# Optimization experiments

Hardware: AMD Instinct MI355X
Metric: run time of the kernel (lower is better)

Reference implementation:

```python
import jax, jax.numpy as jnp
import numpy as np

N_F = 256
NH = 8
D = N_F // NH
TP = (2.0 * D) ** 0.5  # temperature: sqrt(temperature_coeff * d)
N_A = 4096


def setup_inputs() -> dict:
    key = jax.random.key(0)
    ks = jax.random.split(key, 8)
    s = 1.0 / np.sqrt(N_F)
    x = jax.random.normal(ks[0], (1, N_A, N_F), dtype=jnp.float32)
    batch_mask = jax.random.randint(ks[1], (N_A, N_A), 0, 2) > 0  # bool
    Wq = jax.random.normal(ks[2], (N_F, N_F), dtype=jnp.float32) * s
    bq = jax.random.normal(ks[3], (N_F,), dtype=jnp.float32) * s
    Wk = jax.random.normal(ks[4], (N_F, N_F), dtype=jnp.float32) * s
    bk = jax.random.normal(ks[5], (N_F,), dtype=jnp.float32) * s
    Wv = jax.random.normal(ks[6], (N_F, N_F), dtype=jnp.float32) * s
    bv = jax.random.normal(ks[7], (N_F,), dtype=jnp.float32) * s
    return {"x": x, "batch_mask": batch_mask, "Wq": Wq, "bq": bq,
            "Wk": Wk, "bk": bk, "Wv": Wv, "bv": bv}


def reference(x, batch_mask, Wq, bq, Wk, bk, Wv, bv):
    # x: (1, n_a, n_f). torch Linear: y = x @ W.T + b
    n_a = x.shape[1]
    q = (x @ Wq.T + bq).reshape(n_a, NH, D)  # (n_a, nh, d)
    k = (x @ Wk.T + bk).reshape(n_a, NH, D)
    v = (x @ Wv.T + bv).reshape(n_a, NH, D)
    # scores: (nh, n_a, n_a)
    a = jnp.einsum('qhd,khd->hqk', q, k) / TP
    neg = jnp.finfo(a.dtype).min
    a = jnp.where(batch_mask[None, :, :], neg, a)
    alpha = jax.nn.softmax(a, axis=-1)
    out = jnp.einsum('hqk,khd->qhd', alpha, v).reshape(1, n_a, NH * D)
    return out
```

## Files before the change

### kernel.cpp

```cpp
#include <hip/hip_runtime.h>
#include <hip/hip_fp16.h>
#include <cfloat>

#define NA 4096
#define NF 256
#define NH 8
#define DH 32
#define KSPLIT 4
#define CHUNK (NA / KSPLIT)

typedef _Float16 half8_t __attribute__((ext_vector_type(8)));
typedef _Float16 half4_t __attribute__((ext_vector_type(4)));
typedef float f32x4 __attribute__((ext_vector_type(4)));
typedef unsigned long long u64;
typedef unsigned long long u64x2 __attribute__((ext_vector_type(2)));

#define QSCALE 0.1803368800112723f

__global__ __launch_bounds__(256) void cast_kernel(
    const float* __restrict__ x, const float* __restrict__ wq,
    const float* __restrict__ wk, const float* __restrict__ wv,
    _Float16* __restrict__ xh, _Float16* __restrict__ whq,
    _Float16* __restrict__ whk, _Float16* __restrict__ whv) {
  const int XQ = NA * NF / 4;
  const int WQ = NF * NF / 4;
  int i = blockIdx.x * blockDim.x + threadIdx.x;
  const float* src; _Float16* dst; int q;
  if (i < XQ)               { src = x;  dst = xh;  q = i; }
  else if (i < XQ + WQ)     { src = wq; dst = whq; q = i - XQ; }
  else if (i < XQ + 2 * WQ) { src = wk; dst = whk; q = i - XQ - WQ; }
  else if (i < XQ + 3 * WQ) { src = wv; dst = whv; q = i - XQ - 2 * WQ; }
  else return;
  float4 v = *(const float4*)(src + q * 4);
  half4_t h = { (_Float16)v.x, (_Float16)v.y, (_Float16)v.z, (_Float16)v.w };
  *(half4_t*)(dst + q * 4) = h;
}

__global__ __launch_bounds__(512) void pack_mask(
    const int* __restrict__ mask, u64* __restrict__ pm) {
  const int q = blockIdx.x * 8 + (threadIdx.x >> 6);
  const int lane = threadIdx.x & 63;
  const int4* rowv = (const int4*)(mask + (size_t)q * NA);
  u64* dst = pm + (size_t)q * 64;
  for (int G = 0; G < 16; ++G) {
    int4 v = rowv[G * 64 + lane];
    u64 b0 = __ballot(v.x != 0);
    u64 b1 = __ballot(v.y != 0);
    u64 b2 = __ballot(v.z != 0);
    u64 b3 = __ballot(v.w != 0);
    if (lane == 0) {
      u64x2 lo = { b0, b1 };
      u64x2 hi = { b2, b3 };
      *(u64x2*)(dst + G * 4) = lo;
      *(u64x2*)(dst + G * 4 + 2) = hi;
    }
  }
}

__global__ __launch_bounds__(256) void proj_gemm(
    const _Float16* __restrict__ xh,
    const _Float16* __restrict__ whq, const _Float16* __restrict__ whk,
    const _Float16* __restrict__ whv,
    const float* __restrict__ bq, const float* __restrict__ bk,
    const float* __restrict__ bv,
    _Float16* __restrict__ Qh, _Float16* __restrict__ Kh,
    _Float16* __restrict__ Vt) {
  const int wave = threadIdx.x >> 6;
  const int lane = threadIdx.x & 63;
  const int lr = lane & 15;
  const int lg = lane >> 4;
  const int lg4 = lg * 4;
  const int m0 = blockIdx.x * 16;
  const int mat = blockIdx.y >> 2;
  const int n0 = (blockIdx.y & 3) * 64 + wave * 16;
  const _Float16* W = (mat == 0) ? whq : (mat == 1) ? whk : whv;
  const float* bias = (mat == 0) ? bq : (mat == 1) ? bk : bv;

  f32x4 acc = {0.f, 0.f, 0.f, 0.f};
#pragma unroll
  for (int k0 = 0; k0 < NF; k0 += 32) {
    half8_t afrag = *(const half8_t*)(xh + (m0 + lr) * NF + k0 + lg * 8);
    half8_t bfrag = *(const half8_t*)(W + (n0 + lr) * NF + k0 + lg * 8);
    acc = __builtin_amdgcn_mfma_f32_16x16x32_f16(afrag, bfrag, acc, 0, 0, 0);
  }
  const int n = n0 + lr;
  const float b = bias[n];
  const int hh = n >> 5;
  const int dd = n & 31;
  if (mat == 0) {
#pragma unroll
    for (int j = 0; j < 4; j++)
      Qh[((size_t)hh * NA + m0 + lg4 + j) * DH + dd] =
          (_Float16)((acc[j] + b) * QSCALE);
  } else if (mat == 1) {
#pragma unroll
    for (int j = 0; j < 4; j++)
      Kh[((size_t)hh * NA + m0 + lg4 + j) * DH + dd] =
          (_Float16)(acc[j] + b);
  } else {
    half4_t hv = { (_Float16)(acc[0] + b), (_Float16)(acc[1] + b),
                   (_Float16)(acc[2] + b), (_Float16)(acc[3] + b) };
    *(half4_t*)(Vt + (size_t)n * NA + m0 + lg4) = hv;
  }
}

__global__ __launch_bounds__(512) void attn_kernel(
    const _Float16* __restrict__ Qh, const _Float16* __restrict__ Kh,
    const _Float16* __restrict__ Vt, const u64* __restrict__ pm,
    float* __restrict__ part, float* __restrict__ sbuf) {
  __shared__ _Float16 vlds[256 * 64];
  const int tid = threadIdx.x;
  const int h = tid >> 6;
  const int lane = tid & 63;
  const int lq = lane & 15;
  const int lg = lane >> 4;
  const int q0 = blockIdx.x * 16;
  const int kb = blockIdx.y;
  const int k0 = kb * CHUNK;

  const half8_t qfrag = *(const half8_t*)(Qh + ((size_t)h * NA + q0 + lq) * DH + lg * 8);
  const _Float16* Kb = Kh + ((size_t)h * NA + k0) * DH;
  const u64* pmq = pm + (size_t)(q0 + lq) * 64 + kb * 16;

  const int str = tid >> 3;
  const int gx = (tid & 7) ^ (str & 7);
  const _Float16* Vp0 = Vt + (size_t)str * NA + k0 + gx * 8;
  const int wr = str * 64 + (tid & 7) * 8;

  int ro[2][4];
#pragma unroll
  for (int u = 0; u < 2; ++u)
#pragma unroll
    for (int t = 0; t < 4; ++t)
      ro[u][t] = (h * DH + u * 16 + lq) * 64 +
                 (((2 * t + (lg >> 1)) ^ (lq & 7)) << 3) + (lg & 1) * 4;

  const int sh0 = lg, sh1 = lg + 4, sh2 = lg + 8, sh3 = lg + 12;

  f32x4 z = {0.f, 0.f, 0.f, 0.f};
  f32x4 o0 = z, o1 = z;
  float srun = 0.f;

  for (int Gc = 0; Gc < 4; ++Gc) {
    const u64* wp = pmq + Gc * 4;
    u64x2 wa = *(const u64x2*)wp;
    u64x2 wb = *(const u64x2*)(wp + 2);
    const u64 w0 = wa[0], w1 = wa[1], w2 = wb[0], w3 = wb[1];
#pragma unroll
    for (int s = 0; s < 4; ++s) {
      const int kt = Gc * 256 + s * 64;
      half8_t vg0 = *(const half8_t*)(Vp0 + kt);
      half8_t vg1 = *(const half8_t*)(Vp0 + (size_t)64 * NA + kt);
      half8_t vg2 = *(const half8_t*)(Vp0 + (size_t)128 * NA + kt);
      half8_t vg3 = *(const half8_t*)(Vp0 + (size_t)192 * NA + kt);

      half8_t kf0 = *(const half8_t*)(Kb + (size_t)(kt + 0 * 16 + lq) * DH + lg * 8);
      half8_t kf1 = *(const half8_t*)(Kb + (size_t)(kt + 1 * 16 + lq) * DH + lg * 8);
      half8_t kf2 = *(const half8_t*)(Kb + (size_t)(kt + 2 * 16 + lq) * DH + lg * 8);
      half8_t kf3 = *(const half8_t*)(Kb + (size_t)(kt + 3 * 16 + lq) * DH + lg * 8);
      f32x4 st0 = __builtin_amdgcn_mfma_f32_16x16x32_f16(kf0, qfrag, z, 0, 0, 0);
      f32x4 st1 = __builtin_amdgcn_mfma_f32_16x16x32_f16(kf1, qfrag, z, 0, 0, 0);
      f32x4 st2 = __builtin_amdgcn_mfma_f32_16x16x32_f16(kf2, qfrag, z, 0, 0, 0);
      f32x4 st3 = __builtin_amdgcn_mfma_f32_16x16x32_f16(kf3, qfrag, z, 0, 0, 0);

      const unsigned m0s = (unsigned)(w0 >> (16 * s));
      const unsigned m1s = (unsigned)(w1 >> (16 * s));
      const unsigned m2s = (unsigned)(w2 >> (16 * s));
      const unsigned m3s = (unsigned)(w3 >> (16 * s));

      f32x4 e0, e1, e2, e3;
      e0[0] = ((m0s >> sh0) & 1) ? 0.f : __builtin_exp2f(st0[0]);
      e0[1] = ((m1s >> sh0) & 1) ? 0.f : __builtin_exp2f(st0[1]);
      e0[2] = ((m2s >> sh0) & 1) ? 0.f : __builtin_exp2f(st0[2]);
      e0[3] = ((m3s >> sh0) & 1) ? 0.f : __builtin_exp2f(st0[3]);
      e1[0] = ((m0s >> sh1) & 1) ? 0.f : __builtin_exp2f(st1[0]);
      e1[1] = ((m1s >> sh1) & 1) ? 0.f : __builtin_exp2f(st1[1]);
      e1[2] = ((m2s >> sh1) & 1) ? 0.f : __builtin_exp2f(st1[2]);
      e1[3] = ((m3s >> sh1) & 1) ? 0.f : __builtin_exp2f(st1[3]);
      e2[0] = ((m0s >> sh2) & 1) ? 0.f : __builtin_exp2f(st2[0]);
      e2[1] = ((m1s >> sh2) & 1) ? 0.f : __builtin_exp2f(st2[1]);
      e2[2] = ((m2s >> sh2) & 1) ? 0.f : __builtin_exp2f(st2[2]);
      e2[3] = ((m3s >> sh2) & 1) ? 0.f : __builtin_exp2f(st2[3]);
      e3[0] = ((m0s >> sh3) & 1) ? 0.f : __builtin_exp2f(st3[0]);
      e3[1] = ((m1s >> sh3) & 1) ? 0.f : __builtin_exp2f(st3[1]);
      e3[2] = ((m2s >> sh3) & 1) ? 0.f : __builtin_exp2f(st3[2]);
      e3[3] = ((m3s >> sh3) & 1) ? 0.f : __builtin_exp2f(st3[3]);

      srun += (e0[0] + e0[1] + e0[2] + e0[3]) + (e1[0] + e1[1] + e1[2] + e1[3])
            + (e2[0] + e2[1] + e2[2] + e2[3]) + (e3[0] + e3[1] + e3[2] + e3[3]);

      half4_t pt0 = { (_Float16)e0[0], (_Float16)e0[1], (_Float16)e0[2], (_Float16)e0[3] };
      half4_t pt1 = { (_Float16)e1[0], (_Float16)e1[1], (_Float16)e1[2], (_Float16)e1[3] };
      half4_t pt2 = { (_Float16)e2[0], (_Float16)e2[1], (_Float16)e2[2], (_Float16)e2[3] };
      half4_t pt3 = { (_Float16)e3[0], (_Float16)e3[1], (_Float16)e3[2], (_Float16)e3[3] };

      *(half8_t*)&vlds[wr]         = vg0;
      *(half8_t*)&vlds[wr + 4096]  = vg1;
      *(half8_t*)&vlds[wr + 8192]  = vg2;
      *(half8_t*)&vlds[wr + 12288] = vg3;
      __syncthreads();

      half4_t va, vb;
      va = *(const half4_t*)&vlds[ro[0][0]]; vb = *(const half4_t*)&vlds[ro[1][0]];
      o0 = __builtin_amdgcn_mfma_f32_16x16x16f16(va, pt0, o0, 0, 0, 0);
      o1 = __builtin_amdgcn_mfma_f32_16x16x16f16(vb, pt0, o1, 0, 0, 0);
      va = *(const half4_t*)&vlds[ro[0][1]]; vb = *(const half4_t*)&vlds[ro[1][1]];
      o0 = __builtin_amdgcn_mfma_f32_16x16x16f16(va, pt1, o0, 0, 0, 0);
      o1 = __builtin_amdgcn_mfma_f32_16x16x16f16(vb, pt1, o1, 0, 0, 0);
      va = *(const half4_t*)&vlds[ro[0][2]]; vb = *(const half4_t*)&vlds[ro[1][2]];
      o0 = __builtin_amdgcn_mfma_f32_16x16x16f16(va, pt2, o0, 0, 0, 0);
      o1 = __builtin_amdgcn_mfma_f32_16x16x16f16(vb, pt2, o1, 0, 0, 0);
      va = *(const half4_t*)&vlds[ro[0][3]]; vb = *(const half4_t*)&vlds[ro[1][3]];
      o0 = __builtin_amdgcn_mfma_f32_16x16x16f16(va, pt3, o0, 0, 0, 0);
      o1 = __builtin_amdgcn_mfma_f32_16x16x16f16(vb, pt3, o1, 0, 0, 0);
      __syncthreads();
    }
  }

  srun += __shfl_xor(srun, 16);
  srun += __shfl_xor(srun, 32);

  const int pb = (blockIdx.x * KSPLIT + kb) * NH + h;
  float* pp = part + (size_t)pb * 512 + lane * 8;
  float4 w0v = { o0[0], o0[1], o0[2], o0[3] };
  float4 w1v = { o1[0], o1[1], o1[2], o1[3] };
  *(float4*)(pp) = w0v;
  *(float4*)(pp + 4) = w1v;
  if (lg == 0) sbuf[pb * 16 + lq] = srun;
}

__global__ __launch_bounds__(256) void combine_kernel(
    const float* __restrict__ part, const float* __restrict__ sbuf,
    float* __restrict__ out) {
  const int wave = blockIdx.x * 4 + (threadIdx.x >> 6);
  const int qt = wave >> 3;
  const int h = wave & 7;
  const int lane = threadIdx.x & 63;
  const int lq = lane & 15;
  const int lg = lane >> 4;

  float S = 0.f;
  float4 O0 = {0.f, 0.f, 0.f, 0.f}, O1 = {0.f, 0.f, 0.f, 0.f};
#pragma unroll
  for (int kb = 0; kb < KSPLIT; kb++) {
    const int pb = (qt * KSPLIT + kb) * NH + h;
    float4 a0 = *(const float4*)(part + (size_t)pb * 512 + lane * 8);
    float4 a1 = *(const float4*)(part + (size_t)pb * 512 + lane * 8 + 4);
    S += sbuf[pb * 16 + lq];
    O0.x += a0.x; O0.y += a0.y; O0.z += a0.z; O0.w += a0.w;
    O1.x += a1.x; O1.y += a1.y; O1.z += a1.z; O1.w += a1.w;
  }
  const float inv = 1.f / S;
  float* orow = out + (qt * 16 + lq) * NF + h * DH;
  float4 r0 = { O0.x * inv, O0.y * inv, O0.z * inv, O0.w * inv };
  float4 r1 = { O1.x * inv, O1.y * inv, O1.z * inv, O1.w * inv };
  *(float4*)(orow + lg * 4) = r0;
  *(float4*)(orow + 16 + lg * 4) = r1;
}

extern "C" void kernel_launch(void* const* d_in, const int* in_sizes, int n_in,
                              void* d_out, int out_size, void* d_ws, size_t ws_size,
                              hipStream_t stream) {
  const float* x  = (const float*)d_in[0];
  const int* mask = (const int*)d_in[1];
  const float* Wq = (const float*)d_in[2];
  const float* bq = (const float*)d_in[3];
  const float* Wk = (const float*)d_in[4];
  const float* bk = (const float*)d_in[5];
  const float* Wv = (const float*)d_in[6];
  const float* bv = (const float*)d_in[7];
  float* out = (float*)d_out;

  char* ws = (char*)d_ws;
  _Float16* xh = (_Float16*)(ws + 0);
  u64* pm      = (u64*)(ws + 0);
  _Float16* whq = (_Float16*)(ws + 2097152);
  _Float16* whk = (_Float16*)(ws + 2228224);
  _Float16* whv = (_Float16*)(ws + 2359296);
  _Float16* Qh  = (_Float16*)(ws + 2490368);
  _Float16* Kh  = (_Float16*)(ws + 4587520);
  _Float16* Vt  = (_Float16*)(ws + 6684672);
  float* part   = (float*)(ws + 8781824);
  float* sbuf   = (float*)(ws + 25559040);

  cast_kernel<<<1216, 256, 0, stream>>>(x, Wq, Wk, Wv, xh, whq, whk, whv);
  proj_gemm<<<dim3(256, 12), 256, 0, stream>>>(xh, whq, whk, whv, bq, bk, bv,
                                               Qh, Kh, Vt);
  pack_mask<<<512, 512, 0, stream>>>(mask, pm);
  attn_kernel<<<dim3(NA / 16, KSPLIT), 512, 0, stream>>>(Qh, Kh, Vt, pm,
                                                         part, sbuf);
  combine_kernel<<<512, 256, 0, stream>>>(part, sbuf, out);
}
```

Measured before the change: 221.2 us.

## Process two query tiles per attention block and fuse fp16 cast into projection

```diff
diff --git a/kernel.cpp b/kernel.cpp
--- a/kernel.cpp
+++ b/kernel.cpp
@@ -8,33 +8,16 @@
 #define DH 32
 #define KSPLIT 4
 #define CHUNK (NA / KSPLIT)
+#define QBLK 32
 
 typedef _Float16 half8_t __attribute__((ext_vector_type(8)));
 typedef _Float16 half4_t __attribute__((ext_vector_type(4)));
 typedef float f32x4 __attribute__((ext_vector_type(4)));
+typedef float f32x8 __attribute__((ext_vector_type(8)));
 typedef unsigned long long u64;
 typedef unsigned long long u64x2 __attribute__((ext_vector_type(2)));
 
 #define QSCALE 0.1803368800112723f
-
-__global__ __launch_bounds__(256) void cast_kernel(
-    const float* __restrict__ x, const float* __restrict__ wq,
-    const float* __restrict__ wk, const float* __restrict__ wv,
-    _Float16* __restrict__ xh, _Float16* __restrict__ whq,
-    _Float16* __restrict__ whk, _Float16* __restrict__ whv) {
-  const int XQ = NA * NF / 4;
-  const int WQ = NF * NF / 4;
-  int i = blockIdx.x * blockDim.x + threadIdx.x;
-  const float* src; _Float16* dst; int q;
-  if (i < XQ)               { src = x;  dst = xh;  q = i; }
-  else if (i < XQ + WQ)     { src = wq; dst = whq; q = i - XQ; }
-  else if (i < XQ + 2 * WQ) { src = wk; dst = whk; q = i - XQ - WQ; }
-  else if (i < XQ + 3 * WQ) { src = wv; dst = whv; q = i - XQ - 2 * WQ; }
-  else return;
-  float4 v = *(const float4*)(src + q * 4);
-  half4_t h = { (_Float16)v.x, (_Float16)v.y, (_Float16)v.z, (_Float16)v.w };
-  *(half4_t*)(dst + q * 4) = h;
-}
 
 __global__ __launch_bounds__(512) void pack_mask(
     const int* __restrict__ mask, u64* __restrict__ pm) {
@@ -58,29 +41,31 @@
 }
 
 __global__ __launch_bounds__(256) void proj_gemm(
-    const _Float16* __restrict__ xh,
-    const _Float16* __restrict__ whq, const _Float16* __restrict__ whk,
-    const _Float16* __restrict__ whv,
+    const float* __restrict__ x,
+    const float* __restrict__ wq, const float* __restrict__ wk,
+    const float* __restrict__ wv,
     const float* __restrict__ bq, const float* __restrict__ bk,
     const float* __restrict__ bv,
     _Float16* __restrict__ Qh, _Float16* __restrict__ Kh,
     _Float16* __restrict__ Vt) {
-  const int wave = threadIdx.x >> 6;
   const int lane = threadIdx.x & 63;
   const int lr = lane & 15;
   const int lg = lane >> 4;
   const int lg4 = lg * 4;
   const int m0 = blockIdx.x * 16;
   const int mat = blockIdx.y >> 2;
-  const int n0 = (blockIdx.y & 3) * 64 + wave * 16;
-  const _Float16* W = (mat == 0) ? whq : (mat == 1) ? whk : whv;
+  const int n0 = (blockIdx.y & 3) * 64 + (threadIdx.x >> 6) * 16;
+  const float* W = (mat == 0) ? wq : (mat == 1) ? wk : wv;
   const float* bias = (mat == 0) ? bq : (mat == 1) ? bk : bv;
 
   f32x4 acc = {0.f, 0.f, 0.f, 0.f};
 #pragma unroll
   for (int k0 = 0; k0 < NF; k0 += 32) {
-    half8_t afrag = *(const half8_t*)(xh + (m0 + lr) * NF + k0 + lg * 8);
-    half8_t bfrag = *(const half8_t*)(W + (n0 + lr) * NF + k0 + lg * 8);
+    f32x8 af = *(const f32x8*)(x + (size_t)(m0 + lr) * NF + k0 + lg * 8);
+    f32x8 bf = *(const f32x8*)(W + (size_t)(n0 + lr) * NF + k0 + lg * 8);
+    half8_t afrag, bfrag;
+#pragma unroll
+    for (int i = 0; i < 8; ++i) { afrag[i] = (_Float16)af[i]; bfrag[i] = (_Float16)bf[i]; }
     acc = __builtin_amdgcn_mfma_f32_16x16x32_f16(afrag, bfrag, acc, 0, 0, 0);
   }
   const int n = n0 + lr;
@@ -104,7 +89,7 @@
   }
 }
 
-__global__ __launch_bounds__(512) void attn_kernel(
+__global__ __launch_bounds__(512, 4) void attn_kernel(
     const _Float16* __restrict__ Qh, const _Float16* __restrict__ Kh,
     const _Float16* __restrict__ Vt, const u64* __restrict__ pm,
     float* __restrict__ part, float* __restrict__ sbuf) {
@@ -114,13 +99,15 @@
   const int lane = tid & 63;
   const int lq = lane & 15;
   const int lg = lane >> 4;
-  const int q0 = blockIdx.x * 16;
+  const int q0 = blockIdx.x * QBLK;
   const int kb = blockIdx.y;
   const int k0 = kb * CHUNK;
 
-  const half8_t qfrag = *(const half8_t*)(Qh + ((size_t)h * NA + q0 + lq) * DH + lg * 8);
+  const half8_t qfA = *(const half8_t*)(Qh + ((size_t)h * NA + q0 + lq) * DH + lg * 8);
+  const half8_t qfB = *(const half8_t*)(Qh + ((size_t)h * NA + q0 + 16 + lq) * DH + lg * 8);
   const _Float16* Kb = Kh + ((size_t)h * NA + k0) * DH;
-  const u64* pmq = pm + (size_t)(q0 + lq) * 64 + kb * 16;
+  const u64* pmA = pm + (size_t)(q0 + lq) * 64 + kb * 16;
+  const u64* pmB = pm + (size_t)(q0 + 16 + lq) * 64 + kb * 16;
 
   const int str = tid >> 3;
   const int gx = (tid & 7) ^ (str & 7);
@@ -138,14 +125,14 @@
   const int sh0 = lg, sh1 = lg + 4, sh2 = lg + 8, sh3 = lg + 12;
 
   f32x4 z = {0.f, 0.f, 0.f, 0.f};
-  f32x4 o0 = z, o1 = z;
-  float srun = 0.f;
+  f32x4 oA0 = z, oA1 = z, oB0 = z, oB1 = z;
+  float srA = 0.f, srB = 0.f;
 
   for (int Gc = 0; Gc < 4; ++Gc) {
-    const u64* wp = pmq + Gc * 4;
-    u64x2 wa = *(const u64x2*)wp;
-    u64x2 wb = *(const u64x2*)(wp + 2);
-    const u64 w0 = wa[0], w1 = wa[1], w2 = wb[0], w3 = wb[1];
+    u64x2 waA = *(const u64x2*)(pmA + Gc * 4);
+    u64x2 wbA = *(const u64x2*)(pmA + Gc * 4 + 2);
+    u64x2 waB = *(const u64x2*)(pmB + Gc * 4);
+    u64x2 wbB = *(const u64x2*)(pmB + Gc * 4 + 2);
 #pragma unroll
     for (int s = 0; s < 4; ++s) {
       const int kt = Gc * 256 + s * 64;
@@ -158,41 +145,71 @@
       half8_t kf1 = *(const half8_t*)(Kb + (size_t)(kt + 1 * 16 + lq) * DH + lg * 8);
       half8_t kf2 = *(const half8_t*)(Kb + (size_t)(kt + 2 * 16 + lq) * DH + lg * 8);
       half8_t kf3 = *(const half8_t*)(Kb + (size_t)(kt + 3 * 16 + lq) * DH + lg * 8);
-      f32x4 st0 = __builtin_amdgcn_mfma_f32_16x16x32_f16(kf0, qfrag, z, 0, 0, 0);
-      f32x4 st1 = __builtin_amdgcn_mfma_f32_16x16x32_f16(kf1, qfrag, z, 0, 0, 0);
-      f32x4 st2 = __builtin_amdgcn_mfma_f32_16x16x32_f16(kf2, qfrag, z, 0, 0, 0);
-      f32x4 st3 = __builtin_amdgcn_mfma_f32_16x16x32_f16(kf3, qfrag, z, 0, 0, 0);
-
-      const unsigned m0s = (unsigned)(w0 >> (16 * s));
-      const unsigned m1s = (unsigned)(w1 >> (16 * s));
-      const unsigned m2s = (unsigned)(w2 >> (16 * s));
-      const unsigned m3s = (unsigned)(w3 >> (16 * s));
-
-      f32x4 e0, e1, e2, e3;
-      e0[0] = ((m0s >> sh0) & 1) ? 0.f : __builtin_exp2f(st0[0]);
-      e0[1] = ((m1s >> sh0) & 1) ? 0.f : __builtin_exp2f(st0[1]);
-      e0[2] = ((m2s >> sh0) & 1) ? 0.f : __builtin_exp2f(st0[2]);
-      e0[3] = ((m3s >> sh0) & 1) ? 0.f : __builtin_exp2f(st0[3]);
-      e1[0] = ((m0s >> sh1) & 1) ? 0.f : __builtin_exp2f(st1[0]);
-      e1[1] = ((m1s >> sh1) & 1) ? 0.f : __builtin_exp2f(st1[1]);
-      e1[2] = ((m2s >> sh1) & 1) ? 0.f : __builtin_exp2f(st1[2]);
-      e1[3] = ((m3s >> sh1) & 1) ? 0.f : __builtin_exp2f(st1[3]);
-      e2[0] = ((m0s >> sh2) & 1) ? 0.f : __builtin_exp2f(st2[0]);
-      e2[1] = ((m1s >> sh2) & 1) ? 0.f : __builtin_exp2f(st2[1]);
-      e2[2] = ((m2s >> sh2) & 1) ? 0.f : __builtin_exp2f(st2[2]);
-      e2[3] = ((m3s >> sh2) & 1) ? 0.f : __builtin_exp2f(st2[3]);
-      e3[0] = ((m0s >> sh3) & 1) ? 0.f : __builtin_exp2f(st3[0]);
-      e3[1] = ((m1s >> sh3) & 1) ? 0.f : __builtin_exp2f(st3[1]);
-      e3[2] = ((m2s >> sh3) & 1) ? 0.f : __builtin_exp2f(st3[2]);
-      e3[3] = ((m3s >> sh3) & 1) ? 0.f : __builtin_exp2f(st3[3]);
-
-      srun += (e0[0] + e0[1] + e0[2] + e0[3]) + (e1[0] + e1[1] + e1[2] + e1[3])
-            + (e2[0] + e2[1] + e2[2] + e2[3]) + (e3[0] + e3[1] + e3[2] + e3[3]);
-
-      half4_t pt0 = { (_Float16)e0[0], (_Float16)e0[1], (_Float16)e0[2], (_Float16)e0[3] };
-      half4_t pt1 = { (_Float16)e1[0], (_Float16)e1[1], (_Float16)e1[2], (_Float16)e1[3] };
-      half4_t pt2 = { (_Float16)e2[0], (_Float16)e2[1], (_Float16)e2[2], (_Float16)e2[3] };
-      half4_t pt3 = { (_Float16)e3[0], (_Float16)e3[1], (_Float16)e3[2], (_Float16)e3[3] };
+      f32x4 sA0 = __builtin_amdgcn_mfma_f32_16x16x32_f16(kf0, qfA, z, 0, 0, 0);
+      f32x4 sA1 = __builtin_amdgcn_mfma_f32_16x16x32_f16(kf1, qfA, z, 0, 0, 0);
+      f32x4 sA2 = __builtin_amdgcn_mfma_f32_16x16x32_f16(kf2, qfA, z, 0, 0, 0);
+      f32x4 sA3 = __builtin_amdgcn_mfma_f32_16x16x32_f16(kf3, qfA, z, 0, 0, 0);
+      f32x4 sB0 = __builtin_amdgcn_mfma_f32_16x16x32_f16(kf0, qfB, z, 0, 0, 0);
+      f32x4 sB1 = __builtin_amdgcn_mfma_f32_16x16x32_f16(kf1, qfB, z, 0, 0, 0);
+      f32x4 sB2 = __builtin_amdgcn_mfma_f32_16x16x32_f16(kf2, qfB, z, 0, 0, 0);
+      f32x4 sB3 = __builtin_amdgcn_mfma_f32_16x16x32_f16(kf3, qfB, z, 0, 0, 0);
+
+      const unsigned mA0 = (unsigned)(waA[0] >> (16 * s));
+      const unsigned mA1 = (unsigned)(waA[1] >> (16 * s));
+      const unsigned mA2 = (unsigned)(wbA[0] >> (16 * s));
+      const unsigned mA3 = (unsigned)(wbA[1] >> (16 * s));
+      const unsigned mB0 = (unsigned)(waB[0] >> (16 * s));
+      const unsigned mB1 = (unsigned)(waB[1] >> (16 * s));
+      const unsigned mB2 = (unsigned)(wbB[0] >> (16 * s));
+      const unsigned mB3 = (unsigned)(wbB[1] >> (16 * s));
+
+      f32x4 eA0, eA1, eA2, eA3, eB0, eB1, eB2, eB3;
+      eA0[0] = ((mA0 >> sh0) & 1) ? 0.f : __builtin_exp2f(sA0[0]);
+      eA0[1] = ((mA1 >> sh0) & 1) ? 0.f : __builtin_exp2f(sA0[1]);
+      eA0[2] = ((mA2 >> sh0) & 1) ? 0.f : __builtin_exp2f(sA0[2]);
+      eA0[3] = ((mA3 >> sh0) & 1) ? 0.f : __builtin_exp2f(sA0[3]);
+      eA1[0] = ((mA0 >> sh1) & 1) ? 0.f : __builtin_exp2f(sA1[0]);
+      eA1[1] = ((mA1 >> sh1) & 1) ? 0.f : __builtin_exp2f(sA1[1]);
+      eA1[2] = ((mA2 >> sh1) & 1) ? 0.f : __builtin_exp2f(sA1[2]);
+      eA1[3] = ((mA3 >> sh1) & 1) ? 0.f : __builtin_exp2f(sA1[3]);
+      eA2[0] = ((mA0 >> sh2) & 1) ? 0.f : __builtin_exp2f(sA2[0]);
+      eA2[1] = ((mA1 >> sh2) & 1) ? 0.f : __builtin_exp2f(sA2[1]);
+      eA2[2] = ((mA2 >> sh2) & 1) ? 0.f : __builtin_exp2f(sA2[2]);
+      eA2[3] = ((mA3 >> sh2) & 1) ? 0.f : __builtin_exp2f(sA2[3]);
+      eA3[0] = ((mA0 >> sh3) & 1) ? 0.f : __builtin_exp2f(sA3[0]);
+      eA3[1] = ((mA1 >> sh3) & 1) ? 0.f : __builtin_exp2f(sA3[1]);
+      eA3[2] = ((mA2 >> sh3) & 1) ? 0.f : __builtin_exp2f(sA3[2]);
+      eA3[3] = ((mA3 >> sh3) & 1) ? 0.f : __builtin_exp2f(sA3[3]);
+      eB0[0] = ((mB0 >> sh0) & 1) ? 0.f : __builtin_exp2f(sB0[0]);
+      eB0[1] = ((mB1 >> sh0) & 1) ? 0.f : __builtin_exp2f(sB0[1]);
+      eB0[2] = ((mB2 >> sh0) & 1) ? 0.f : __builtin_exp2f(sB0[2]);
+      eB0[3] = ((mB3 >> sh0) & 1) ? 0.f : __builtin_exp2f(sB0[3]);
+      eB1[0] = ((mB0 >> sh1) & 1) ? 0.f : __builtin_exp2f(sB1[0]);
+      eB1[1] = ((mB1 >> sh1) & 1) ? 0.f : __builtin_exp2f(sB1[1]);
+      eB1[2] = ((mB2 >> sh1) & 1) ? 0.f : __builtin_exp2f(sB1[2]);
+      eB1[3] = ((mB3 >> sh1) & 1) ? 0.f : __builtin_exp2f(sB1[3]);
+      eB2[0] = ((mB0 >> sh2) & 1) ? 0.f : __builtin_exp2f(sB2[0]);
+      eB2[1] = ((mB1 >> sh2) & 1) ? 0.f : __builtin_exp2f(sB2[1]);
+      eB2[2] = ((mB2 >> sh2) & 1) ? 0.f : __builtin_exp2f(sB2[2]);
+      eB2[3] = ((mB3 >> sh2) & 1) ? 0.f : __builtin_exp2f(sB2[3]);
+      eB3[0] = ((mB0 >> sh3) & 1) ? 0.f : __builtin_exp2f(sB3[0]);
+      eB3[1] = ((mB1 >> sh3) & 1) ? 0.f : __builtin_exp2f(sB3[1]);
+      eB3[2] = ((mB2 >> sh3) & 1) ? 0.f : __builtin_exp2f(sB3[2]);
+      eB3[3] = ((mB3 >> sh3) & 1) ? 0.f : __builtin_exp2f(sB3[3]);
+
+      srA += (eA0[0] + eA0[1] + eA0[2] + eA0[3]) + (eA1[0] + eA1[1] + eA1[2] + eA1[3])
+           + (eA2[0] + eA2[1] + eA2[2] + eA2[3]) + (eA3[0] + eA3[1] + eA3[2] + eA3[3]);
+      srB += (eB0[0] + eB0[1] + eB0[2] + eB0[3]) + (eB1[0] + eB1[1] + eB1[2] + eB1[3])
+           + (eB2[0] + eB2[1] + eB2[2] + eB2[3]) + (eB3[0] + eB3[1] + eB3[2] + eB3[3]);
+
+      half4_t pA0 = { (_Float16)eA0[0], (_Float16)eA0[1], (_Float16)eA0[2], (_Float16)eA0[3] };
+      half4_t pA1 = { (_Float16)eA1[0], (_Float16)eA1[1], (_Float16)eA1[2], (_Float16)eA1[3] };
+      half4_t pA2 = { (_Float16)eA2[0], (_Float16)eA2[1], (_Float16)eA2[2], (_Float16)eA2[3] };
+      half4_t pA3 = { (_Float16)eA3[0], (_Float16)eA3[1], (_Float16)eA3[2], (_Float16)eA3[3] };
+      half4_t pB0 = { (_Float16)eB0[0], (_Float16)eB0[1], (_Float16)eB0[2], (_Float16)eB0[3] };
+      half4_t pB1 = { (_Float16)eB1[0], (_Float16)eB1[1], (_Float16)eB1[2], (_Float16)eB1[3] };
+      half4_t pB2 = { (_Float16)eB2[0], (_Float16)eB2[1], (_Float16)eB2[2], (_Float16)eB2[3] };
+      half4_t pB3 = { (_Float16)eB3[0], (_Float16)eB3[1], (_Float16)eB3[2], (_Float16)eB3[3] };
 
       *(half8_t*)&vlds[wr]         = vg0;
       *(half8_t*)&vlds[wr + 4096]  = vg1;
@@ -202,31 +219,42 @@
 
       half4_t va, vb;
       va = *(const half4_t*)&vlds[ro[0][0]]; vb = *(const half4_t*)&vlds[ro[1][0]];
-      o0 = __builtin_amdgcn_mfma_f32_16x16x16f16(va, pt0, o0, 0, 0, 0);
-      o1 = __builtin_amdgcn_mfma_f32_16x16x16f16(vb, pt0, o1, 0, 0, 0);
+      oA0 = __builtin_amdgcn_mfma_f32_16x16x16f16(va, pA0, oA0, 0, 0, 0);
+      oA1 = __builtin_amdgcn_mfma_f32_16x16x16f16(vb, pA0, oA1, 0, 0, 0);
+      oB0 = __builtin_amdgcn_mfma_f32_16x16x16f16(va, pB0, oB0, 0, 0, 0);
+      oB1 = __builtin_amdgcn_mfma_f32_16x16x16f16(vb, pB0, oB1, 0, 0, 0);
       va = *(const half4_t*)&vlds[ro[0][1]]; vb = *(const half4_t*)&vlds[ro[1][1]];
-      o0 = __builtin_amdgcn_mfma_f32_16x16x16f16(va, pt1, o0, 0, 0, 0);
-      o1 = __builtin_amdgcn_mfma_f32_16x16x16f16(vb, pt1, o1, 0, 0, 0);
+      oA0 = __builtin_amdgcn_mfma_f32_16x16x16f16(va, pA1, oA0, 0, 0, 0);
+      oA1 = __builtin_amdgcn_mfma_f32_16x16x16f16(vb, pA1, oA1, 0, 0, 0);
+      oB0 = __builtin_amdgcn_mfma_f32_16x16x16f16(va, pB1, oB0, 0, 0, 0);
+      oB1 = __builtin_amdgcn_mfma_f32_16x16x16f16(vb, pB1, oB1, 0, 0, 0);
       va = *(const half4_t*)&vlds[ro[0][2]]; vb = *(const half4_t*)&vlds[ro[1][2]];
-      o0 = __builtin_amdgcn_mfma_f32_16x16x16f16(va, pt2, o0, 0, 0, 0);
-      o1 = __builtin_amdgcn_mfma_f32_16x16x16f16(vb, pt2, o1, 0, 0, 0);
+      oA0 = __builtin_amdgcn_mfma_f32_16x16x16f16(va, pA2, oA0, 0, 0, 0);
+      oA1 = __builtin_amdgcn_mfma_f32_16x16x16f16(vb, pA2, oA1, 0, 0, 0);
+      oB0 = __builtin_amdgcn_mfma_f32_16x16x16f16(va, pB2, oB0, 0, 0, 0);
+      oB1 = __builtin_amdgcn_mfma_f32_16x16x16f16(vb, pB2, oB1, 0, 0, 0);
       va = *(const half4_t*)&vlds[ro[0][3]]; vb = *(const half4_t*)&vlds[ro[1][3]];
-      o0 = __builtin_amdgcn_mfma_f32_16x16x16f16(va, pt3, o0, 0, 0, 0);
-      o1 = __builtin_amdgcn_mfma_f32_16x16x16f16(vb, pt3, o1, 0, 0, 0);
+      oA0 = __builtin_amdgcn_mfma_f32_16x16x16f16(va, pA3, oA0, 0, 0, 0);
+      oA1 = __builtin_amdgcn_mfma_f32_16x16x16f16(vb, pA3, oA1, 0, 0, 0);
+      oB0 = __builtin_amdgcn_mfma_f32_16x16x16f16(va, pB3, oB0, 0, 0, 0);
+      oB1 = __builtin_amdgcn_mfma_f32_16x16x16f16(vb, pB3, oB1, 0, 0, 0);
       __syncthreads();
     }
   }
 
-  srun += __shfl_xor(srun, 16);
-  srun += __shfl_xor(srun, 32);
+  srA += __shfl_xor(srA, 16); srA += __shfl_xor(srA, 32);
+  srB += __shfl_xor(srB, 16); srB += __shfl_xor(srB, 32);
 
   const int pb = (blockIdx.x * KSPLIT + kb) * NH + h;
-  float* pp = part + (size_t)pb * 512 + lane * 8;
-  float4 w0v = { o0[0], o0[1], o0[2], o0[3] };
-  float4 w1v = { o1[0], o1[1], o1[2], o1[3] };
-  *(float4*)(pp) = w0v;
-  *(float4*)(pp + 4) = w1v;
-  if (lg == 0) sbuf[pb * 16 + lq] = srun;
+  float* pp = part + (size_t)pb * 1024 + lane * 8;
+  *(float4*)(pp)           = (float4){ oA0[0], oA0[1], oA0[2], oA0[3] };
+  *(float4*)(pp + 4)       = (float4){ oA1[0], oA1[1], oA1[2], oA1[3] };
+  *(float4*)(pp + 512)     = (float4){ oB0[0], oB0[1], oB0[2], oB0[3] };
+  *(float4*)(pp + 516)     = (float4){ oB1[0], oB1[1], oB1[2], oB1[3] };
+  if (lg == 0) {
+    sbuf[pb * 32 + lq] = srA;
+    sbuf[pb * 32 + 16 + lq] = srB;
+  }
 }
 
 __global__ __launch_bounds__(256) void combine_kernel(
@@ -239,23 +267,30 @@
   const int lq = lane & 15;
   const int lg = lane >> 4;
 
-  float S = 0.f;
-  float4 O0 = {0.f, 0.f, 0.f, 0.f}, O1 = {0.f, 0.f, 0.f, 0.f};
+  float SA = 0.f, SB = 0.f;
+  float4 A0 = {0,0,0,0}, A1 = {0,0,0,0}, B0 = {0,0,0,0}, B1 = {0,0,0,0};
 #pragma unroll
   for (int kb = 0; kb < KSPLIT; kb++) {
     const int pb = (qt * KSPLIT + kb) * NH + h;
-    float4 a0 = *(const float4*)(part + (size_t)pb * 512 + lane * 8);
-    float4 a1 = *(const float4*)(part + (size_t)pb * 512 + lane * 8 + 4);
-    S += sbuf[pb * 16 + lq];
-    O0.x += a0.x; O0.y += a0.y; O0.z += a0.z; O0.w += a0.w;
-    O1.x += a1.x; O1.y += a1.y; O1.z += a1.z; O1.w += a1.w;
-  }
-  const float inv = 1.f / S;
-  float* orow = out + (qt * 16 + lq) * NF + h * DH;
-  float4 r0 = { O0.x * inv, O0.y * inv, O0.z * inv, O0.w * inv };
-  float4 r1 = { O1.x * inv, O1.y * inv, O1.z * inv, O1.w * inv };
-  *(float4*)(orow + lg * 4) = r0;
-  *(float4*)(orow + 16 + lg * 4) = r1;
+    const float* pp = part + (size_t)pb * 1024 + lane * 8;
+    float4 a0 = *(const float4*)(pp);
+    float4 a1 = *(const float4*)(pp + 4);
+    float4 b0 = *(const float4*)(pp + 512);
+    float4 b1 = *(const float4*)(pp + 516);
+    SA += sbuf[pb * 32 + lq];
+    SB += sbuf[pb * 32 + 16 + lq];
+    A0.x += a0.x; A0.y += a0.y; A0.z += a0.z; A0.w += a0.w;
+    A1.x += a1.x; A1.y += a1.y; A1.z += a1.z; A1.w += a1.w;
+    B0.x += b0.x; B0.y += b0.y; B0.z += b0.z; B0.w += b0.w;
+    B1.x += b1.x; B1.y += b1.y; B1.z += b1.z; B1.w += b1.w;
+  }
+  const float iA = 1.f / SA, iB = 1.f / SB;
+  float* rowA = out + (size_t)(qt * QBLK + lq) * NF + h * DH;
+  float* rowB = out + (size_t)(qt * QBLK + 16 + lq) * NF + h * DH;
+  *(float4*)(rowA + lg * 4)      = (float4){ A0.x * iA, A0.y * iA, A0.z * iA, A0.w * iA };
+  *(float4*)(rowA + 16 + lg * 4) = (float4){ A1.x * iA, A1.y * iA, A1.z * iA, A1.w * iA };
+  *(float4*)(rowB + lg * 4)      = (float4){ B0.x * iB, B0.y * iB, B0.z * iB, B0.w * iB };
+  *(float4*)(rowB + 16 + lg * 4) = (float4){ B1.x * iB, B1.y * iB, B1.z * iB, B1.w * iB };
 }
 
 extern "C" void kernel_launch(void* const* d_in, const int* in_sizes, int n_in,
@@ -272,22 +307,17 @@
   float* out = (float*)d_out;
 
   char* ws = (char*)d_ws;
-  _Float16* xh = (_Float16*)(ws + 0);
-  u64* pm      = (u64*)(ws + 0);
-  _Float16* whq = (_Float16*)(ws + 2097152);
-  _Float16* whk = (_Float16*)(ws + 2228224);
-  _Float16* whv = (_Float16*)(ws + 2359296);
-  _Float16* Qh  = (_Float16*)(ws + 2490368);
-  _Float16* Kh  = (_Float16*)(ws + 4587520);
-  _Float16* Vt  = (_Float16*)(ws + 6684672);
-  float* part   = (float*)(ws + 8781824);
-  float* sbuf   = (float*)(ws + 25559040);
-
-  cast_kernel<<<1216, 256, 0, stream>>>(x, Wq, Wk, Wv, xh, whq, whk, whv);
-  proj_gemm<<<dim3(256, 12), 256, 0, stream>>>(xh, whq, whk, whv, bq, bk, bv,
+  u64* pm       = (u64*)(ws + 0);
+  _Float16* Qh  = (_Float16*)(ws + 2097152);
+  _Float16* Kh  = (_Float16*)(ws + 4194304);
+  _Float16* Vt  = (_Float16*)(ws + 6291456);
+  float* part   = (float*)(ws + 8388608);
+  float* sbuf   = (float*)(ws + 25165824);
+
+  proj_gemm<<<dim3(256, 12), 256, 0, stream>>>(x, Wq, Wk, Wv, bq, bk, bv,
                                                Qh, Kh, Vt);
   pack_mask<<<512, 512, 0, stream>>>(mask, pm);
-  attn_kernel<<<dim3(NA / 16, KSPLIT), 512, 0, stream>>>(Qh, Kh, Vt, pm,
-                                                         part, sbuf);
-  combine_kernel<<<512, 256, 0, stream>>>(part, sbuf, out);
-}
+  attn_kernel<<<dim3(NA / QBLK, KSPLIT), 512, 0, stream>>>(Qh, Kh, Vt, pm,
+                                                           part, sbuf);
+  combine_kernel<<<256, 256, 0, stream>>>(part, sbuf, out);
+}
```

After: 301.8 us. +36.4%, slower.
